# Optimization experiments

Measured on AMD Instinct MI355X. Metric: run time of the kernel, lower is better.

The kernel has to match this reference:

```python
import jax, jax.numpy as jnp
import numpy as np

N = 100000   # nodes
E = 1600000  # edges (nnz of adj_mat)
D = 64       # dim
EPS = 1e-6
SLOPE = 0.2  # tf.nn.leaky_relu default alpha


def _layernorm(x, g, b):
    mu = jnp.mean(x, axis=-1, keepdims=True)
    var = jnp.mean(jnp.square(x - mu), axis=-1, keepdims=True)
    return (x - mu) * jax.lax.rsqrt(var + EPS) * g + b


def setup_inputs() -> dict:
    key = jax.random.key(0)
    ks = jax.random.split(key, 8)
    scale = 0.05
    return {
        "query": jax.random.normal(ks[0], (N, D), dtype=jnp.float32),
        "input_": jax.random.normal(ks[1], (N, D), dtype=jnp.float32),
        "edge_row": jnp.sort(jax.random.randint(ks[2], (E,), 0, N)),
        "edge_col": jax.random.randint(ks[3], (E,), 0, N),
        "Ww": jax.random.normal(ks[4], (D, D), dtype=jnp.float32) * scale,
        "Wb": jnp.zeros((D,), jnp.float32),
        "W1w": jax.random.normal(ks[5], (D, D), dtype=jnp.float32) * scale,
        "W1b": jnp.zeros((D,), jnp.float32),
        "W2w": jax.random.normal(ks[6], (D, D), dtype=jnp.float32) * scale,
        "W2b": jnp.zeros((D,), jnp.float32),
        "g1": jnp.ones((D,), jnp.float32),
        "b1": jnp.zeros((D,), jnp.float32),
        "g2": jnp.ones((D,), jnp.float32),
        "b2": jnp.zeros((D,), jnp.float32),
    }


def reference(query, input_, edge_row, edge_col, Ww, Wb, W1w, W1b, W2w, W2b, g1, b1, g2, b2):
    # layernorm1 + dense projections
    x = _layernorm(input_, g1, b1)                       # [N, D]
    dense = x @ Ww + Wb                                  # [N, D]
    at1 = query @ W1w + W1b                              # [N, D]
    at2 = x @ W2w + W2b                                  # [N, D]
    # per-node scalar scores (sum over feature axis), tanh; dropout is identity in eval
    s1 = jnp.tanh(jnp.sum(at1 * query, axis=1))          # [N] row-side score
    s2 = jnp.tanh(jnp.sum(at2 * x, axis=1))              # [N] col-side score
    # edge logits: leaky_relu(s1[i] + s2[j]) for each edge (i, j); adj values are 1
    logits = jax.nn.leaky_relu(s1[edge_row] + s2[edge_col], negative_slope=SLOPE)  # [E]
    # sparse softmax per destination row (over that row's nonzeros)
    row_max = jax.ops.segment_max(logits, edge_row, num_segments=N)   # [N]
    ex = jnp.exp(logits - row_max[edge_row])                          # [E]
    denom = jax.ops.segment_sum(ex, edge_row, num_segments=N)         # [N]
    attn = ex / denom[edge_row]                                       # [E]
    # SpMM: out[i] = sum_j attn_ij * dense[j]
    out = jax.ops.segment_sum(attn[:, None] * dense[edge_col], edge_row, num_segments=N)  # [N, D]
    return _layernorm(out, g2, b2)
```

## Files before the change

### kernel.cpp

```cpp
#include <hip/hip_runtime.h>
#include <math.h>

#define D 64
#define EPS 1e-6f
#define SLOPE 0.2f

typedef _Float16 f16;
typedef _Float16 f16x4 __attribute__((ext_vector_type(4)));
typedef _Float16 f16x8 __attribute__((ext_vector_type(8)));
typedef float f32x4 __attribute__((ext_vector_type(4)));

__device__ __forceinline__ float red4(float v) {
  v += __shfl_xor(v, 16, 64);
  v += __shfl_xor(v, 32, 64);
  return v;
}
__device__ __forceinline__ float leaky(float l) {
  return (l > 0.f) ? l : SLOPE * l;
}
__device__ __forceinline__ float bperm_f(int byte_addr, float v) {
  return __int_as_float(
      __builtin_amdgcn_ds_bpermute(byte_addr, __float_as_int(v)));
}
__device__ __forceinline__ int bperm_i(int byte_addr, int v) {
  return __builtin_amdgcn_ds_bpermute(byte_addr, v);
}

__global__ void wprep_kernel(const float* __restrict__ Ww,
                             const float* __restrict__ W1w,
                             const float* __restrict__ W2w,
                             f16* __restrict__ wt)
{
  int i = blockIdx.x * blockDim.x + threadIdx.x;
  if (i >= 3 * 4096) return;
  int mat = i >> 12, idx = i & 4095;
  int n = idx >> 6, k = idx & 63;
  const float* src = (mat == 0) ? Ww : (mat == 1) ? W1w : W2w;
  int t = n >> 4, mloc = n & 15;
  int c = k >> 4, grp = (k >> 2) & 3, j = k & 3;
  int frag = mat * 16 + t * 4 + c;
  int lane = grp * 16 + mloc;
  wt[(frag << 8) + (lane << 2) + j] = (f16)src[k * 64 + n];
}

__global__ __launch_bounds__(256, 2) void node_kernel(
    const float* __restrict__ query, const float* __restrict__ input_,
    const f16* __restrict__ wt,
    const float* __restrict__ Wb,  const float* __restrict__ W1b,
    const float* __restrict__ W2b,
    const float* __restrict__ g1,  const float* __restrict__ b1,
    f16* __restrict__ dense_h, float* __restrict__ s1, float* __restrict__ s2,
    int N)
{
  const int lane = threadIdx.x & 63;
  const int grp  = lane >> 4;
  const int mloc = lane & 15;
  const int wave  = blockIdx.x * (blockDim.x >> 6) + (threadIdx.x >> 6);
  const int nwav  = gridDim.x * (blockDim.x >> 6);
  const int TILES = (N + 15) >> 4;

  f16x4 wd[4][4], w1r[4][4], w2r[4][4];
#pragma unroll
  for (int t = 0; t < 4; ++t)
#pragma unroll
    for (int c = 0; c < 4; ++c) {
      int f = t * 4 + c;
      wd[t][c]  = *(const f16x4*)(wt + ((f)      << 8) + (lane << 2));
      w1r[t][c] = *(const f16x4*)(wt + ((16 + f) << 8) + (lane << 2));
      w2r[t][c] = *(const f16x4*)(wt + ((32 + f) << 8) + (lane << 2));
    }
  f32x4 gk[4], bk[4];
#pragma unroll
  for (int c = 0; c < 4; ++c) {
    gk[c] = *(const f32x4*)(g1 + c * 16 + grp * 4);
    bk[c] = *(const f32x4*)(b1 + c * 16 + grp * 4);
  }
  float wbr[4];
#pragma unroll
  for (int t = 0; t < 4; ++t) wbr[t] = Wb[t * 16 + mloc];

  auto prefetch = [&](f32x4* QB, f32x4* IB, int tl) {
    int m = tl * 16 + mloc;
    bool v = (tl < TILES) && (m < N);
    size_t b = (size_t)m * D;
#pragma unroll
    for (int c = 0; c < 4; ++c) {
      int k0 = c * 16 + grp * 4;
      if (v) {
        QB[c] = *(const f32x4*)(query + b + k0);
        IB[c] = *(const f32x4*)(input_ + b + k0);
      } else {
        QB[c] = (f32x4){0.f, 0.f, 0.f, 0.f};
        IB[c] = (f32x4){0.f, 0.f, 0.f, 0.f};
      }
    }
  };

  auto process = [&](f32x4* QB, f32x4* IB, int tl) {
    float s = 0.f;
#pragma unroll
    for (int c = 0; c < 4; ++c)
#pragma unroll
      for (int j = 0; j < 4; ++j) s += IB[c][j];
    s = red4(s);
    float mu = s * (1.f / D);
    float v2 = 0.f;
#pragma unroll
    for (int c = 0; c < 4; ++c)
#pragma unroll
      for (int j = 0; j < 4; ++j) {
        float d = IB[c][j] - mu;
        v2 += d * d;
      }
    v2 = red4(v2);
    float rs = rsqrtf(v2 * (1.f / D) + EPS);

    f16x4 xh[4], qh[4];
#pragma unroll
    for (int c = 0; c < 4; ++c)
#pragma unroll
      for (int j = 0; j < 4; ++j) {
        xh[c][j] = (f16)((IB[c][j] - mu) * rs * gk[c][j] + bk[c][j]);
        qh[c][j] = (f16)QB[c][j];
      }

    const int m  = tl * 16 + mloc;
    const bool mv = (m < N);

#pragma unroll
    for (int t = 0; t < 4; ++t) {
      f32x4 acc = {0.f, 0.f, 0.f, 0.f};
#pragma unroll
      for (int c = 0; c < 4; ++c)
        acc = __builtin_amdgcn_mfma_f32_16x16x16f16(xh[c], wd[t][c], acc, 0, 0, 0);
#pragma unroll
      for (int r = 0; r < 4; ++r) {
        int row = tl * 16 + grp * 4 + r;
        if (row < N)
          dense_h[(size_t)row * D + t * 16 + mloc] = (f16)(acc[r] + wbr[t]);
      }
    }

    float dot1 = 0.f, dot2 = 0.f;
#pragma unroll
    for (int t = 0; t < 4; ++t) {
      f32x4 a1 = {0.f, 0.f, 0.f, 0.f}, a2 = {0.f, 0.f, 0.f, 0.f};
#pragma unroll
      for (int c = 0; c < 4; ++c) {
        a1 = __builtin_amdgcn_mfma_f32_16x16x16f16(w1r[t][c], qh[c], a1, 0, 0, 0);
        a2 = __builtin_amdgcn_mfma_f32_16x16x16f16(w2r[t][c], xh[c], a2, 0, 0, 0);
      }
      f32x4 b1v = *(const f32x4*)(W1b + t * 16 + grp * 4);
      f32x4 b2v = *(const f32x4*)(W2b + t * 16 + grp * 4);
#pragma unroll
      for (int r = 0; r < 4; ++r) {
        dot1 += (a1[r] + b1v[r]) * (float)qh[t][r];
        dot2 += (a2[r] + b2v[r]) * (float)xh[t][r];
      }
    }
    dot1 = red4(dot1);
    dot2 = red4(dot2);
    if (grp == 0 && mv) {
      s1[m] = tanhf(dot1);
      s2[m] = tanhf(dot2);
    }
  };

  f32x4 qA[4], iA[4], qB[4], iB[4];
  int tl = wave;
  prefetch(qA, iA, tl);
  while (tl < TILES) {
    prefetch(qB, iB, tl + nwav);
    process(qA, iA, tl);
    tl += nwav;
    if (tl >= TILES) break;
    prefetch(qA, iA, tl + nwav);
    process(qB, iB, tl);
    tl += nwav;
  }
}

__global__ void rowptr_kernel(const int* __restrict__ erow,
                              int* __restrict__ row_ptr, int E, int N)
{
  int e = blockIdx.x * blockDim.x + threadIdx.x;
  if (e >= E) return;
  int r = erow[e];
  if (e == 0) {
    for (int rr = 0; rr <= r; ++rr) row_ptr[rr] = 0;
  } else {
    int rp = erow[e - 1];
    for (int rr = rp + 1; rr <= r; ++rr) row_ptr[rr] = e;
  }
  if (e == E - 1) {
    for (int rr = r + 1; rr <= N; ++rr) row_ptr[rr] = E;
  }
}

template <int NIT>
__device__ __forceinline__ void accum(const f16* __restrict__ dense_h,
                                      int eg, int fl, int c, float w,
                                      float* A)
{
#pragma unroll
  for (int it = 0; it < NIT; ++it) {
    int a = (((eg & 4) << 3) + (it << 2) + (eg & 3)) << 2;
    float wb = bperm_f(a, w);
    int   cb = bperm_i(a, c);
    f16x8 v = *(const f16x8*)(dense_h + (size_t)cb * D + (fl << 3));
#pragma unroll
    for (int j = 0; j < 8; ++j)
      A[j] = fmaf((float)v[j], wb, A[j]);
  }
}

__global__ __launch_bounds__(256) void edge_kernel(
    const int* __restrict__ row_ptr, const int* __restrict__ ecol,
    const float* __restrict__ s1v, const float* __restrict__ s2v,
    const f16* __restrict__ dense_h,
    const float* __restrict__ g2, const float* __restrict__ b2,
    float* __restrict__ out, int N)
{
  const int lane = threadIdx.x & 63;
  const int eg   = lane >> 3;
  const int fl   = lane & 7;
  const int wv   = blockIdx.x * (blockDim.x >> 6) + (threadIdx.x >> 6);
  const int r0   = wv << 1;
  const int r1   = r0 + 1;
  if (r0 >= N) return;

  const int pa = row_ptr[r0];
  const int pb = row_ptr[r0 + 1];
  const int pc = row_ptr[min(r0 + 2, N)];
  const int d0 = pb - pa;
  const int d1 = (r1 < N) ? (pc - pb) : 0;

  const bool hi  = (lane >= 32);
  const int  sl  = lane & 31;
  const int  dgx = hi ? d1 : d0;
  const int  bse = hi ? pb : pa;
  const float s1x = s1v[hi ? min(r1, N - 1) : r0];

  int c = 0;
  if (sl < dgx) c = ecol[bse + sl];
  float w = 0.f;
  if (sl < dgx) w = __expf(leaky(s1x + s2v[c]));

  float A[8] = {0.f, 0.f, 0.f, 0.f, 0.f, 0.f, 0.f, 0.f};
  const int maxd = max(d0, d1);

  if (maxd <= 32) {
    const int nit = (maxd + 3) >> 2;
    if      (nit <= 2) accum<2>(dense_h, eg, fl, c, w, A);
    else if (nit <= 4) accum<4>(dense_h, eg, fl, c, w, A);
    else if (nit <= 6) accum<6>(dense_h, eg, fl, c, w, A);
    else               accum<8>(dense_h, eg, fl, c, w, A);
  } else {
    float A0[8] = {0.f, 0.f, 0.f, 0.f, 0.f, 0.f, 0.f, 0.f};
    float A1[8] = {0.f, 0.f, 0.f, 0.f, 0.f, 0.f, 0.f, 0.f};
    auto rowacc = [&](int st, int en, float s1i, float* Ar) {
      for (int b = st; b < en; b += 64) {
        int nb = min(64, en - b);
        int cc = 0;
        float ww = 0.f;
        if (lane < nb) {
          cc = ecol[b + lane];
          ww = __expf(leaky(s1i + s2v[cc]));
        }
#pragma unroll
        for (int it = 0; it < 8; ++it) {
          int a = ((it << 3) + eg) << 2;
          float wb = bperm_f(a, ww);
          int   cb = bperm_i(a, cc);
          f16x8 v = *(const f16x8*)(dense_h + (size_t)cb * D + (fl << 3));
#pragma unroll
          for (int j = 0; j < 8; ++j)
            Ar[j] = fmaf((float)v[j], wb, Ar[j]);
        }
      }
    };
    rowacc(pa, pb, s1v[r0], A0);
    if (r1 < N) rowacc(pb, pc, s1v[r1], A1);
#pragma unroll
    for (int j = 0; j < 8; ++j) {
      A0[j] += __shfl_xor(A0[j], 32, 64);
      A1[j] += __shfl_xor(A1[j], 32, 64);
      A[j] = hi ? A1[j] : A0[j];
    }
  }

#pragma unroll
  for (int j = 0; j < 8; ++j) {
    A[j] += __shfl_xor(A[j], 8, 64);
    A[j] += __shfl_xor(A[j], 16, 64);
  }

  float sa = 0.f, sq = 0.f;
#pragma unroll
  for (int j = 0; j < 8; ++j) {
    sa += A[j];
    sq += A[j] * A[j];
  }
#pragma unroll
  for (int m = 4; m > 0; m >>= 1) {
    sa += __shfl_xor(sa, m, 64);
    sq += __shfl_xor(sq, m, 64);
  }
  float mu  = sa * (1.f / D);
  float var = fmaxf(sq * (1.f / D) - mu * mu, 0.f);
  float rs  = rsqrtf(var + EPS);

  f32x4 gv0 = *(const f32x4*)(g2 + (fl << 3));
  f32x4 gv1 = *(const f32x4*)(g2 + (fl << 3) + 4);
  f32x4 bv0 = *(const f32x4*)(b2 + (fl << 3));
  f32x4 bv1 = *(const f32x4*)(b2 + (fl << 3) + 4);

  f32x4 o0, o1;
#pragma unroll
  for (int j = 0; j < 4; ++j) {
    o0[j] = (A[j]     - mu) * rs * gv0[j] + bv0[j];
    o1[j] = (A[j + 4] - mu) * rs * gv1[j] + bv1[j];
  }
  if (eg == 0) {
    *(f32x4*)(out + (size_t)r0 * D + (fl << 3))     = o0;
    *(f32x4*)(out + (size_t)r0 * D + (fl << 3) + 4) = o1;
  } else if (eg == 4 && r1 < N) {
    *(f32x4*)(out + (size_t)r1 * D + (fl << 3))     = o0;
    *(f32x4*)(out + (size_t)r1 * D + (fl << 3) + 4) = o1;
  }
}

extern "C" void kernel_launch(void* const* d_in, const int* in_sizes, int n_in,
                              void* d_out, int out_size, void* d_ws, size_t ws_size,
                              hipStream_t stream)
{
  const float* query  = (const float*)d_in[0];
  const float* input_ = (const float*)d_in[1];
  const int*   erow   = (const int*)d_in[2];
  const int*   ecol   = (const int*)d_in[3];
  const float* Ww     = (const float*)d_in[4];
  const float* Wb     = (const float*)d_in[5];
  const float* W1w    = (const float*)d_in[6];
  const float* W1b    = (const float*)d_in[7];
  const float* W2w    = (const float*)d_in[8];
  const float* W2b    = (const float*)d_in[9];
  const float* g1     = (const float*)d_in[10];
  const float* b1     = (const float*)d_in[11];
  const float* g2     = (const float*)d_in[12];
  const float* b2     = (const float*)d_in[13];

  const int N = in_sizes[0] / D;
  const int E = in_sizes[2];
  float* out = (float*)d_out;

  char* ws = (char*)d_ws;
  f16*   dense_h = (f16*)ws;
  float* s1      = (float*)(ws + (size_t)N * D * sizeof(f16));
  float* s2      = s1 + N;
  int*   row_ptr = (int*)(s2 + N);
  uintptr_t wtp  = (uintptr_t)(row_ptr + N + 1);
  wtp = (wtp + 15) & ~(uintptr_t)15;
  f16* wt = (f16*)wtp;

  wprep_kernel<<<(3 * 4096 + 255) / 256, 256, 0, stream>>>(Ww, W1w, W2w, wt);
  node_kernel<<<512, 256, 0, stream>>>(query, input_, wt, Wb, W1b,
                                       W2b, g1, b1, dense_h, s1, s2, N);
  rowptr_kernel<<<(E + 255) / 256, 256, 0, stream>>>(erow, row_ptr, E, N);
  const int waves = (N + 1) / 2;
  edge_kernel<<<(waves + 3) / 4, 256, 0, stream>>>(row_ptr, ecol, s1, s2,
                                                   dense_h, g2, b2, out, N);
}
```

Before: 75.06 us.

## Make edge kernel persistent with software-pipelined prefetch of next row pair

The edge kernel becomes a grid-stride persistent loop over row pairs, launched with a fixed grid of 2048 blocks. Row pointers, column indices and edge weights for the next pair are loaded while the current pair is gathered and normalized, to hide load latency. The layernorm gamma/beta loads are hoisted out of the loop, and the node kernel grid is doubled. In exchange, register pressure rises from the double-buffered state, and fewer resident waves may reduce latency hiding from occupancy.

```diff
diff --git a/kernel.cpp b/kernel.cpp
--- a/kernel.cpp
+++ b/kernel.cpp
@@ -219,114 +219,138 @@
     const float* __restrict__ s1v, const float* __restrict__ s2v,
     const f16* __restrict__ dense_h,
     const float* __restrict__ g2, const float* __restrict__ b2,
-    float* __restrict__ out, int N)
+    float* __restrict__ out, int N, int npairs)
 {
   const int lane = threadIdx.x & 63;
   const int eg   = lane >> 3;
   const int fl   = lane & 7;
-  const int wv   = blockIdx.x * (blockDim.x >> 6) + (threadIdx.x >> 6);
-  const int r0   = wv << 1;
-  const int r1   = r0 + 1;
-  if (r0 >= N) return;
-
-  const int pa = row_ptr[r0];
-  const int pb = row_ptr[r0 + 1];
-  const int pc = row_ptr[min(r0 + 2, N)];
-  const int d0 = pb - pa;
-  const int d1 = (r1 < N) ? (pc - pb) : 0;
-
   const bool hi  = (lane >= 32);
   const int  sl  = lane & 31;
-  const int  dgx = hi ? d1 : d0;
-  const int  bse = hi ? pb : pa;
-  const float s1x = s1v[hi ? min(r1, N - 1) : r0];
-
-  int c = 0;
-  if (sl < dgx) c = ecol[bse + sl];
-  float w = 0.f;
-  if (sl < dgx) w = __expf(leaky(s1x + s2v[c]));
-
-  float A[8] = {0.f, 0.f, 0.f, 0.f, 0.f, 0.f, 0.f, 0.f};
-  const int maxd = max(d0, d1);
-
-  if (maxd <= 32) {
-    const int nit = (maxd + 3) >> 2;
-    if      (nit <= 2) accum<2>(dense_h, eg, fl, c, w, A);
-    else if (nit <= 4) accum<4>(dense_h, eg, fl, c, w, A);
-    else if (nit <= 6) accum<6>(dense_h, eg, fl, c, w, A);
-    else               accum<8>(dense_h, eg, fl, c, w, A);
-  } else {
-    float A0[8] = {0.f, 0.f, 0.f, 0.f, 0.f, 0.f, 0.f, 0.f};
-    float A1[8] = {0.f, 0.f, 0.f, 0.f, 0.f, 0.f, 0.f, 0.f};
-    auto rowacc = [&](int st, int en, float s1i, float* Ar) {
-      for (int b = st; b < en; b += 64) {
-        int nb = min(64, en - b);
-        int cc = 0;
-        float ww = 0.f;
-        if (lane < nb) {
-          cc = ecol[b + lane];
-          ww = __expf(leaky(s1i + s2v[cc]));
+  const int wv0  = blockIdx.x * (blockDim.x >> 6) + (threadIdx.x >> 6);
+  const int nwav = gridDim.x * (blockDim.x >> 6);
+
+  const f32x4 gv0 = *(const f32x4*)(g2 + (fl << 3));
+  const f32x4 gv1 = *(const f32x4*)(g2 + (fl << 3) + 4);
+  const f32x4 bv0 = *(const f32x4*)(b2 + (fl << 3));
+  const f32x4 bv1 = *(const f32x4*)(b2 + (fl << 3) + 4);
+
+  auto prologue = [&](int pv, int& c, float& w, int& d0, int& d1,
+                      int& pa, int& pb, int& pc) {
+    c = 0; w = 0.f; d0 = 0; d1 = 0; pa = 0; pb = 0; pc = 0;
+    if (pv >= npairs) return;
+    int r0 = pv << 1;
+    pa = row_ptr[r0];
+    pb = row_ptr[r0 + 1];
+    pc = row_ptr[min(r0 + 2, N)];
+    d0 = pb - pa;
+    d1 = (r0 + 1 < N) ? (pc - pb) : 0;
+    int dgx = hi ? d1 : d0;
+    int bse = hi ? pb : pa;
+    float s1x = s1v[min(r0 + (hi ? 1 : 0), N - 1)];
+    if (sl < dgx) {
+      c = ecol[bse + sl];
+      w = __expf(leaky(s1x + s2v[c]));
+    }
+  };
+
+  auto process = [&](int pv, int c, float w, int d0, int d1,
+                     int pa, int pb, int pc) {
+    if (pv >= npairs) return;
+    const int r0 = pv << 1;
+    const int r1 = r0 + 1;
+    float A[8] = {0.f, 0.f, 0.f, 0.f, 0.f, 0.f, 0.f, 0.f};
+    const int maxd = max(d0, d1);
+
+    if (maxd <= 32) {
+      const int nit = (maxd + 3) >> 2;
+      if      (nit <= 2) accum<2>(dense_h, eg, fl, c, w, A);
+      else if (nit <= 4) accum<4>(dense_h, eg, fl, c, w, A);
+      else if (nit <= 6) accum<6>(dense_h, eg, fl, c, w, A);
+      else               accum<8>(dense_h, eg, fl, c, w, A);
+    } else {
+      float A0[8] = {0.f, 0.f, 0.f, 0.f, 0.f, 0.f, 0.f, 0.f};
+      float A1[8] = {0.f, 0.f, 0.f, 0.f, 0.f, 0.f, 0.f, 0.f};
+      auto rowacc = [&](int st, int en, float s1i, float* Ar) {
+        for (int b = st; b < en; b += 64) {
+          int nb = min(64, en - b);
+          int cc = 0;
+          float ww = 0.f;
+          if (lane < nb) {
+            cc = ecol[b + lane];
+            ww = __expf(leaky(s1i + s2v[cc]));
+          }
+#pragma unroll
+          for (int it = 0; it < 8; ++it) {
+            int a = ((it << 3) + eg) << 2;
+            float wb = bperm_f(a, ww);
+            int   cb = bperm_i(a, cc);
+            f16x8 v = *(const f16x8*)(dense_h + (size_t)cb * D + (fl << 3));
+#pragma unroll
+            for (int j = 0; j < 8; ++j)
+              Ar[j] = fmaf((float)v[j], wb, Ar[j]);
+          }
         }
-#pragma unroll
-        for (int it = 0; it < 8; ++it) {
-          int a = ((it << 3) + eg) << 2;
-          float wb = bperm_f(a, ww);
-          int   cb = bperm_i(a, cc);
-          f16x8 v = *(const f16x8*)(dense_h + (size_t)cb * D + (fl << 3));
-#pragma unroll
-          for (int j = 0; j < 8; ++j)
-            Ar[j] = fmaf((float)v[j], wb, Ar[j]);
-        }
-      }
-    };
-    rowacc(pa, pb, s1v[r0], A0);
-    if (r1 < N) rowacc(pb, pc, s1v[r1], A1);
+      };
+      rowacc(pa, pb, s1v[r0], A0);
+      if (r1 < N) rowacc(pb, pc, s1v[r1], A1);
+#pragma unroll
+      for (int j = 0; j < 8; ++j) {
+        A0[j] += __shfl_xor(A0[j], 32, 64);
+        A1[j] += __shfl_xor(A1[j], 32, 64);
+        A[j] = hi ? A1[j] : A0[j];
+      }
+    }
+
 #pragma unroll
     for (int j = 0; j < 8; ++j) {
-      A0[j] += __shfl_xor(A0[j], 32, 64);
-      A1[j] += __shfl_xor(A1[j], 32, 64);
-      A[j] = hi ? A1[j] : A0[j];
-    }
-  }
-
-#pragma unroll
-  for (int j = 0; j < 8; ++j) {
-    A[j] += __shfl_xor(A[j], 8, 64);
-    A[j] += __shfl_xor(A[j], 16, 64);
-  }
-
-  float sa = 0.f, sq = 0.f;
-#pragma unroll
-  for (int j = 0; j < 8; ++j) {
-    sa += A[j];
-    sq += A[j] * A[j];
-  }
-#pragma unroll
-  for (int m = 4; m > 0; m >>= 1) {
-    sa += __shfl_xor(sa, m, 64);
-    sq += __shfl_xor(sq, m, 64);
-  }
-  float mu  = sa * (1.f / D);
-  float var = fmaxf(sq * (1.f / D) - mu * mu, 0.f);
-  float rs  = rsqrtf(var + EPS);
-
-  f32x4 gv0 = *(const f32x4*)(g2 + (fl << 3));
-  f32x4 gv1 = *(const f32x4*)(g2 + (fl << 3) + 4);
-  f32x4 bv0 = *(const f32x4*)(b2 + (fl << 3));
-  f32x4 bv1 = *(const f32x4*)(b2 + (fl << 3) + 4);
-
-  f32x4 o0, o1;
-#pragma unroll
-  for (int j = 0; j < 4; ++j) {
-    o0[j] = (A[j]     - mu) * rs * gv0[j] + bv0[j];
-    o1[j] = (A[j + 4] - mu) * rs * gv1[j] + bv1[j];
-  }
-  if (eg == 0) {
-    *(f32x4*)(out + (size_t)r0 * D + (fl << 3))     = o0;
-    *(f32x4*)(out + (size_t)r0 * D + (fl << 3) + 4) = o1;
-  } else if (eg == 4 && r1 < N) {
-    *(f32x4*)(out + (size_t)r1 * D + (fl << 3))     = o0;
-    *(f32x4*)(out + (size_t)r1 * D + (fl << 3) + 4) = o1;
+      A[j] += __shfl_xor(A[j], 8, 64);
+      A[j] += __shfl_xor(A[j], 16, 64);
+    }
+
+    float sa = 0.f, sq = 0.f;
+#pragma unroll
+    for (int j = 0; j < 8; ++j) {
+      sa += A[j];
+      sq += A[j] * A[j];
+    }
+#pragma unroll
+    for (int m = 4; m > 0; m >>= 1) {
+      sa += __shfl_xor(sa, m, 64);
+      sq += __shfl_xor(sq, m, 64);
+    }
+    float mu  = sa * (1.f / D);
+    float var = fmaxf(sq * (1.f / D) - mu * mu, 0.f);
+    float rs  = rsqrtf(var + EPS);
+
+    f32x4 o0, o1;
+#pragma unroll
+    for (int j = 0; j < 4; ++j) {
+      o0[j] = (A[j]     - mu) * rs * gv0[j] + bv0[j];
+      o1[j] = (A[j + 4] - mu) * rs * gv1[j] + bv1[j];
+    }
+    if (eg == 0) {
+      *(f32x4*)(out + (size_t)r0 * D + (fl << 3))     = o0;
+      *(f32x4*)(out + (size_t)r0 * D + (fl << 3) + 4) = o1;
+    } else if (eg == 4 && r1 < N) {
+      *(f32x4*)(out + (size_t)r1 * D + (fl << 3))     = o0;
+      *(f32x4*)(out + (size_t)r1 * D + (fl << 3) + 4) = o1;
+    }
+  };
+
+  int cA, d0A, d1A, paA, pbA, pcA;
+  int cB, d0B, d1B, paB, pbB, pcB;
+  float wA, wB;
+
+  int pv = wv0;
+  prologue(pv, cA, wA, d0A, d1A, paA, pbA, pcA);
+  while (pv < npairs) {
+    prologue(pv + nwav, cB, wB, d0B, d1B, paB, pbB, pcB);
+    process(pv, cA, wA, d0A, d1A, paA, pbA, pcA);
+    pv += nwav;
+    if (pv >= npairs) break;
+    prologue(pv + nwav, cA, wA, d0A, d1A, paA, pbA, pcA);
+    process(pv, cB, wB, d0B, d1B, paB, pbB, pcB);
+    pv += nwav;
   }
 }
 
@@ -363,10 +387,10 @@
   f16* wt = (f16*)wtp;
 
   wprep_kernel<<<(3 * 4096 + 255) / 256, 256, 0, stream>>>(Ww, W1w, W2w, wt);
-  node_kernel<<<512, 256, 0, stream>>>(query, input_, wt, Wb, W1b,
-                                       W2b, g1, b1, dense_h, s1, s2, N);
+  node_kernel<<<1024, 256, 0, stream>>>(query, input_, wt, Wb, W1b,
+                                        W2b, g1, b1, dense_h, s1, s2, N);
   rowptr_kernel<<<(E + 255) / 256, 256, 0, stream>>>(erow, row_ptr, E, N);
-  const int waves = (N + 1) / 2;
-  edge_kernel<<<(waves + 3) / 4, 256, 0, stream>>>(row_ptr, ecol, s1, s2,
-                                                   dense_h, g2, b2, out, N);
-}
+  const int npairs = (N + 1) / 2;
+  edge_kernel<<<2048, 256, 0, stream>>>(row_ptr, ecol, s1, s2,
+                                        dense_h, g2, b2, out, N, npairs);
+}
```

Measured after the change: 77.61 us. 3.4% more time.
